# Kernel optimization log

Measured on AMD Instinct MI355X. Metric: run time of the kernel, lower is better.

Reference implementation:

```python
import jax, jax.numpy as jnp
import numpy as np

N, L, C, H, W, HEAD = 16, 256, 512, 32, 32, 16

def setup_inputs() -> dict:
    key = jax.random.key(0)
    ks = jax.random.split(key, 8)
    s = 0.02  # weight init scale
    return {
        "feature": jax.random.normal(ks[0], (N, C, H, W), jnp.float32),
        "token": jax.random.normal(ks[1], (N, L, C), jnp.float32),
        "wq": jax.random.normal(ks[2], (C, C), jnp.float32) * s,
        "bq": jax.random.normal(ks[3], (C,), jnp.float32) * s,
        "wk": jax.random.normal(ks[4], (C, C), jnp.float32) * s,
        "bk": jax.random.normal(ks[5], (C,), jnp.float32) * s,
        "wv": jax.random.normal(ks[6], (C, C), jnp.float32) * s,
        "bv": jax.random.normal(ks[7], (C,), jnp.float32) * s,
    }

def reference(feature, token, wq, bq, wk, bk, wv, bv):
    n, c, hgt, wid = feature.shape
    h = HEAD
    d = c // h
    l = token.shape[1]
    scale = jnp.asarray(np.sqrt(c / h), feature.dtype)
    tok = token.transpose(0, 2, 1)  # (N, C, L)
    # 1x1 conv projections == per-position GEMMs
    v = (jnp.einsum('ncl,dc->ndl', tok, wv) + bv[None, :, None]).reshape(n, h, d, l)
    k = (jnp.einsum('ncl,dc->ndl', tok, wk) + bk[None, :, None]).reshape(n, h, d, l)
    q = (jnp.einsum('nchw,dc->ndhw', feature, wq) + bq[None, :, None, None])
    q = q.reshape(n, h, d, hgt * wid).transpose(0, 1, 3, 2)  # (N, h, HW, d)
    scores = jnp.einsum('nhqd,nhdl->nhql', q, k) / scale  # (N, h, HW, L)
    coef = jax.nn.softmax(scores, axis=-1)
    proj = jnp.einsum('nhdl,nhql->nhdq', v, coef)  # (N, h, d, HW)
    return feature + proj.reshape(n, c, hgt, wid)
```

## Files before the change

### kernel.cpp

```cpp
#include <hip/hip_runtime.h>
#include <hip/hip_bf16.h>

#define N_ 16
#define L_ 256
#define C_ 512
#define HW_ 1024
#define HEADS_ 16
#define DH_ 32

typedef unsigned short u16;
typedef unsigned int u32;
typedef __attribute__((ext_vector_type(8))) short short8_t;
typedef __attribute__((ext_vector_type(4))) float f32x4;
typedef __attribute__((ext_vector_type(2))) unsigned int u32x2;

__device__ __forceinline__ u16 f2bs(float f) {
    union { float f; u32 i; } x; x.f = f;
    u32 r = x.i + 0x7fffu + ((x.i >> 16) & 1u);
    return (u16)(r >> 16);
}
__device__ __forceinline__ u32 cvt_pk_bf16(float lo, float hi) {
    u32 r;
    asm("v_cvt_pk_bf16_f32 %0, %1, %2" : "=v"(r) : "v"(lo), "v"(hi));
    return r;
}
#define AS1(p) (const __attribute__((address_space(1))) void*)(p)
#define AS3(p) (__attribute__((address_space(3))) void*)(p)

__global__ __launch_bounds__(256) void prep_kernel(
    const float* __restrict__ token, const float* __restrict__ wq,
    const float* __restrict__ wk, const float* __restrict__ wv,
    u16* __restrict__ tokb, u16* __restrict__ wqb,
    u16* __restrict__ wkb, u16* __restrict__ wvb)
{
    const int idx = blockIdx.x * 256 + threadIdx.x;
    const float* s; u16* d; int off;
    if (idx < 524288)            { s = token; d = tokb; off = idx; }
    else if (idx < 524288+65536) { s = wq; d = wqb; off = idx - 524288; }
    else if (idx < 524288+131072){ s = wk; d = wkb; off = idx - 524288 - 65536; }
    else                         { s = wv; d = wvb; off = idx - 524288 - 131072; }
    float4 v = ((const float4*)s)[off];
    ushort4 w;
    w.x = f2bs(v.x); w.y = f2bs(v.y); w.z = f2bs(v.z); w.w = f2bs(v.w);
    ((ushort4*)d)[off] = w;
}

__global__ __launch_bounds__(256) void proj_kernel(
    const float* __restrict__ feature,
    const u16* __restrict__ tokb, const u16* __restrict__ wqb,
    const u16* __restrict__ wkb, const u16* __restrict__ wvb,
    const float* __restrict__ bq, const float* __restrict__ bk,
    const float* __restrict__ bv,
    u16* __restrict__ Qout, u16* __restrict__ Kout, u16* __restrict__ Vt)
{
    __shared__ __align__(16) unsigned char smem[53248];

    const int t = threadIdx.x;
    const int lane = t & 63, wid = t >> 6;
    const int i16 = lane & 15, g = lane >> 4;

    if (blockIdx.x < 256) {
        const int xcd = blockIdx.x & 7, j = blockIdx.x >> 3;
        const int m0 = (xcd * 4 + (j & 3)) * 128;
        const int n0 = (j >> 2) * 64;
        u16* Tok = (u16*)smem;
        u16* Bk  = (u16*)(smem + 16384);
        u16* Bv  = (u16*)(smem + 24576);
        u16 (*LTo)[72] = (u16(*)[72])smem;

        const int wm = wid >> 1, wn = wid & 1;
        const int r8 = t >> 3, gr = t & 7;

        f32x4 ak[4][2], av[4][2];
        #pragma unroll
        for (int mt = 0; mt < 4; ++mt)
            #pragma unroll
            for (int nt = 0; nt < 2; ++nt) {
                ak[mt][nt] = (f32x4){0.f, 0.f, 0.f, 0.f};
                av[mt][nt] = (f32x4){0.f, 0.f, 0.f, 0.f};
            }

        for (int c0 = 0; c0 < C_; c0 += 64) {
            __syncthreads();
            #pragma unroll
            for (int p = 0; p < 4; ++p) {
                const int row = p * 32 + r8;
                __builtin_amdgcn_global_load_lds(
                    AS1(tokb + (size_t)(m0 + row) * C_ + c0 + ((gr ^ (row & 7)) << 3)),
                    AS3(smem + (p * 32 + wid * 8) * 128), 16, 0, 0);
            }
            #pragma unroll
            for (int p = 0; p < 2; ++p) {
                const int row = p * 32 + r8;
                const int gs = (gr ^ (row & 7)) << 3;
                __builtin_amdgcn_global_load_lds(
                    AS1(wkb + (size_t)(n0 + row) * C_ + c0 + gs),
                    AS3(smem + 16384 + (p * 32 + wid * 8) * 128), 16, 0, 0);
                __builtin_amdgcn_global_load_lds(
                    AS1(wvb + (size_t)(n0 + row) * C_ + c0 + gs),
                    AS3(smem + 24576 + (p * 32 + wid * 8) * 128), 16, 0, 0);
            }
            __syncthreads();
            #pragma unroll
            for (int ks = 0; ks < 2; ++ks) {
                short8_t a[4], bbk[2], bbv[2];
                #pragma unroll
                for (int mt = 0; mt < 4; ++mt) {
                    const int m = wm * 64 + mt * 16 + i16;
                    a[mt] = *(const short8_t*)&Tok[m * 64 + ((((ks << 2) | g) ^ (m & 7)) << 3)];
                }
                #pragma unroll
                for (int nt = 0; nt < 2; ++nt) {
                    const int d = wn * 32 + nt * 16 + i16;
                    const int sw = d * 64 + ((((ks << 2) | g) ^ (d & 7)) << 3);
                    bbk[nt] = *(const short8_t*)&Bk[sw];
                    bbv[nt] = *(const short8_t*)&Bv[sw];
                }
                #pragma unroll
                for (int mt = 0; mt < 4; ++mt)
                    #pragma unroll
                    for (int nt = 0; nt < 2; ++nt) {
                        ak[mt][nt] = __builtin_amdgcn_mfma_f32_16x16x32_bf16(
                            a[mt], bbk[nt], ak[mt][nt], 0, 0, 0);
                        av[mt][nt] = __builtin_amdgcn_mfma_f32_16x16x32_bf16(
                            a[mt], bbv[nt], av[mt][nt], 0, 0, 0);
                    }
            }
        }
        const int nb = m0 >> 8, l0 = m0 & 255;
        const size_t vtbase = (size_t)nb * C_ * L_;
        #pragma unroll
        for (int nt = 0; nt < 2; ++nt) {
            const int d = n0 + wn * 32 + nt * 16 + i16;
            const float bb = bv[d];
            #pragma unroll
            for (int mt = 0; mt < 4; ++mt) {
                ushort4 w;
                w.x = f2bs(av[mt][nt][0] + bb);
                w.y = f2bs(av[mt][nt][1] + bb);
                w.z = f2bs(av[mt][nt][2] + bb);
                w.w = f2bs(av[mt][nt][3] + bb);
                const int l = l0 + wm * 64 + mt * 16 + g * 4;
                *(ushort4*)&Vt[vtbase + (size_t)d * L_ + l] = w;
            }
        }
        __syncthreads();
        #pragma unroll
        for (int nt = 0; nt < 2; ++nt) {
            const int col = wn * 32 + nt * 16 + i16;
            const float bb = bk[n0 + col];
            #pragma unroll
            for (int mt = 0; mt < 4; ++mt)
                #pragma unroll
                for (int r = 0; r < 4; ++r)
                    LTo[wm * 64 + mt * 16 + g * 4 + r][col] = f2bs(ak[mt][nt][r] + bb);
        }
        __syncthreads();
        #pragma unroll
        for (int rep = 0; rep < 4; ++rep) {
            const int m = (t >> 3) + rep * 32;
            const int cs = (t & 7) * 8;
            *(short8_t*)&Kout[(size_t)(m0 + m) * C_ + n0 + cs] = *(short8_t*)&LTo[m][cs];
        }
    } else {
        const int qid = blockIdx.x - 256;
        const int xcd = qid & 7, loc = qid >> 3;
        const int mtile = xcd * 32 + (loc >> 2);
        const int nt4 = loc & 3;
        const int m0 = mtile * 64;
        const int n0 = nt4 * 128;
        const int n = m0 >> 10, pos0 = m0 & (HW_ - 1);
        const u32 FEAT0 = 32768;

        const int wq_d = wid & 1, wq_pos = wid >> 1;
        const int r8 = t >> 3, gr = t & 7;
        const int frow = t >> 2, fpb = t & 3;

        f32x4 acc[4][2];
        #pragma unroll
        for (int dm = 0; dm < 4; ++dm)
            #pragma unroll
            for (int pf = 0; pf < 2; ++pf)
                acc[dm][pf] = (f32x4){0.f, 0.f, 0.f, 0.f};

        float f[16];

        #define QF_LOADFEAT(c) { \
            const float* src = &feature[((size_t)n * C_ + (c) * 64 + frow) * HW_ + pos0 + fpb * 16]; \
            *(float4*)&f[0]  = *(const float4*)&src[0];  \
            *(float4*)&f[4]  = *(const float4*)&src[4];  \
            *(float4*)&f[8]  = *(const float4*)&src[8];  \
            *(float4*)&f[12] = *(const float4*)&src[12]; }
        #define QF_STAGEWQ(c, buf) { \
            _Pragma("unroll") \
            for (int p = 0; p < 4; ++p) { \
                const int row = p * 32 + r8; \
                __builtin_amdgcn_global_load_lds( \
                    AS1(wqb + (size_t)(n0 + row) * C_ + (c) * 64 + ((gr ^ (row & 7)) << 3)), \
                    AS3(smem + (buf) * 16384 + (p * 32 + wid * 8) * 128), 16, 0, 0); } }
        #define QF_WRITEFEAT(buf) { \
            u32 pw[8]; \
            _Pragma("unroll") \
            for (int k2 = 0; k2 < 8; ++k2) pw[k2] = cvt_pk_bf16(f[2*k2], f[2*k2+1]); \
            unsigned char* dst = smem + FEAT0 + (buf) * 10240 + \
                (u32)(((frow >> 2) * 4 + fpb) * 160 + (frow & 3) * 32); \
            *(short8_t*)dst = *(short8_t*)&pw[0]; \
            *(short8_t*)(dst + 16) = *(short8_t*)&pw[4]; }

        QF_LOADFEAT(0);
        QF_STAGEWQ(0, 0);
        QF_WRITEFEAT(0);
        __syncthreads();

        for (int c = 0; c < 8; ++c) {
            const int cur = c & 1;
            if (c < 7) {
                QF_LOADFEAT(c + 1);
                QF_STAGEWQ(c + 1, cur ^ 1);
            }
            short8_t a2[2][4], b2[2][2];
            #pragma unroll
            for (int ks = 0; ks < 2; ++ks)
                #pragma unroll
                for (int dm = 0; dm < 4; ++dm) {
                    const int m = wq_d * 64 + dm * 16 + i16;
                    a2[ks][dm] = *(const short8_t*)(smem + cur * 16384 +
                        (u32)(m * 128 + ((((ks << 2) | g) ^ (m & 7)) << 4)));
                }
            #pragma unroll
            for (int ks = 0; ks < 2; ++ks)
                #pragma unroll
                for (int pf = 0; pf < 2; ++pf) {
                    const int pb = wq_pos * 2 + pf;
                    const u32 vaddr = FEAT0 + cur * 10240 +
                        (u32)(((ks * 8 + g * 2) * 4 + pb) * 160) + (u32)i16 * 2;
                    u32x2 lo, hi;
                    asm volatile("ds_read_b64_tr_b16 %0, %1" : "=v"(lo) : "v"(vaddr));
                    asm volatile("ds_read_b64_tr_b16 %0, %1 offset:640" : "=v"(hi) : "v"(vaddr));
                    union { u32 w[4]; short8_t v; } pk;
                    pk.w[0] = lo[0]; pk.w[1] = lo[1];
                    pk.w[2] = hi[0]; pk.w[3] = hi[1];
                    b2[ks][pf] = pk.v;
                }
            asm volatile("s_waitcnt lgkmcnt(0)" ::: "memory");
            __builtin_amdgcn_sched_barrier(0);
            #pragma unroll
            for (int ks = 0; ks < 2; ++ks)
                #pragma unroll
                for (int dm = 0; dm < 4; ++dm)
                    #pragma unroll
                    for (int pf = 0; pf < 2; ++pf)
                        acc[dm][pf] = __builtin_amdgcn_mfma_f32_16x16x32_bf16(
                            a2[ks][dm], b2[ks][pf], acc[dm][pf], 0, 0, 0);
            if (c < 7) QF_WRITEFEAT(cur ^ 1);
            __syncthreads();
        }
        #pragma unroll
        for (int dm = 0; dm < 4; ++dm) {
            const int dbase = wq_d * 64 + dm * 16 + g * 4;
            float4 b4 = *(const float4*)&bq[n0 + dbase];
            const float bb[4] = {b4.x, b4.y, b4.z, b4.w};
            #pragma unroll
            for (int pf = 0; pf < 2; ++pf) {
                const int pos = wq_pos * 32 + pf * 16 + i16;
                ushort4 w;
                w.x = f2bs(acc[dm][pf][0] + bb[0]);
                w.y = f2bs(acc[dm][pf][1] + bb[1]);
                w.z = f2bs(acc[dm][pf][2] + bb[2]);
                w.w = f2bs(acc[dm][pf][3] + bb[3]);
                *(ushort4*)&Qout[(size_t)(m0 + pos) * C_ + n0 + dbase] = w;
            }
        }
    }
}

__global__ __launch_bounds__(256) void attn_kernel(
    const u16* __restrict__ Qws, const u16* __restrict__ Kws,
    const u16* __restrict__ Vws, const float* __restrict__ feature,
    float* __restrict__ out)
{
    __shared__ __align__(16) unsigned char smem[32768];

    const int t = threadIdx.x;
    const int wid = t >> 6, lane = t & 63;
    const int i16 = lane & 15, g = lane >> 4;
    const int pt = blockIdx.x, h = blockIdx.y, n = blockIdx.z;
    const int pos0 = pt * 64;
    const size_t qbase = ((size_t)n * HW_ + pos0) * C_ + h * DH_;
    const size_t kbase = ((size_t)n * L_) * C_ + h * DH_;
    const size_t vbase = (size_t)n * C_ * L_ + (size_t)h * DH_ * L_;

    const int q = wid * 16 + i16;

    short8_t bq = *(const short8_t*)&Qws[qbase + (size_t)q * C_ + g * 8];

    #pragma unroll
    for (int p = 0; p < 4; ++p) {
        const int kg = (lane & 3) ^ ((lane >> 3) & 3);
        const int kr = wid * 64 + p * 16 + (lane >> 2);
        const u16* ksrc = Kws + kbase + (size_t)kr * C_ + kg * 8;
        __builtin_amdgcn_global_load_lds(AS1(ksrc),
            AS3(smem + wid * 4096 + p * 1024), 16, 0, 0);
        const int vd = wid * 8 + p * 2 + (lane >> 5);
        const u16* vsrc = Vws + vbase + (size_t)vd * L_ + ((lane & 31) ^ (vd & 7)) * 8;
        __builtin_amdgcn_global_load_lds(AS1(vsrc),
            AS3(smem + 16384 + wid * 4096 + p * 1024), 16, 0, 0);
    }
    __syncthreads();

    const int kgr = g ^ ((i16 >> 1) & 3);
    f32x4 s[16];
    #pragma unroll
    for (int nf = 0; nf < 16; ++nf) {
        short8_t a = *(const short8_t*)(smem + (nf * 16 + i16) * 64 + kgr * 16);
        f32x4 z = {0.f, 0.f, 0.f, 0.f};
        s[nf] = __builtin_amdgcn_mfma_f32_16x16x32_bf16(a, bq, z, 0, 0, 0);
    }

    float mm[16], sm[16];
    #pragma unroll
    for (int nf = 0; nf < 16; ++nf)
        mm[nf] = fmaxf(fmaxf(s[nf][0], s[nf][1]), fmaxf(s[nf][2], s[nf][3]));
    #pragma unroll
    for (int st = 8; st >= 1; st >>= 1)
        #pragma unroll
        for (int i = 0; i < 8; ++i)
            if (i < st) mm[i] = fmaxf(mm[i], mm[i + st]);
    float m = mm[0];
    m = fmaxf(m, __shfl_xor(m, 16));
    m = fmaxf(m, __shfl_xor(m, 32));

    const float K2 = 0.25506288f;
    #pragma unroll
    for (int nf = 0; nf < 16; ++nf) {
        #pragma unroll
        for (int r = 0; r < 4; ++r) s[nf][r] = exp2f((s[nf][r] - m) * K2);
        sm[nf] = (s[nf][0] + s[nf][1]) + (s[nf][2] + s[nf][3]);
    }
    #pragma unroll
    for (int st = 8; st >= 1; st >>= 1)
        #pragma unroll
        for (int i = 0; i < 8; ++i)
            if (i < st) sm[i] += sm[i + st];
    float ssum = sm[0];
    ssum += __shfl_xor(ssum, 16);
    ssum += __shfl_xor(ssum, 32);
    const float pinv = 1.0f / ssum;

    __syncthreads();

    f32x4 o0 = {0.f, 0.f, 0.f, 0.f}, o1 = {0.f, 0.f, 0.f, 0.f};
    const int e7 = i16 & 7;

    #pragma unroll
    for (int hb = 0; hb < 2; ++hb) {
        #pragma unroll
        for (int nfp = 0; nfp < 8; ++nfp) {
            const int nf = hb * 8 + nfp;
            #pragma unroll
            for (int w = 0; w < 2; ++w) {
                u32 pw = cvt_pk_bf16(s[nf][2 * w] * pinv, s[nf][2 * w + 1] * pinv);
                const int gran = (nfp * 2 + (g >> 1)) ^ e7;
                *(u32*)(smem + q * 256 + gran * 16 + ((g & 1) * 2 + w) * 4) = pw;
            }
        }
        __syncthreads();
        #pragma unroll
        for (int ks = 0; ks < 4; ++ks) {
            short8_t pb = *(const short8_t*)(smem + q * 256 + (((ks * 4 + g) ^ e7) * 16));
            const int vg = (((hb * 4 + ks) * 4 + g) ^ e7) * 16;
            short8_t va0 = *(const short8_t*)(smem + 16384 + i16 * 512 + vg);
            short8_t va1 = *(const short8_t*)(smem + 16384 + (16 + i16) * 512 + vg);
            o0 = __builtin_amdgcn_mfma_f32_16x16x32_bf16(va0, pb, o0, 0, 0, 0);
            o1 = __builtin_amdgcn_mfma_f32_16x16x32_bf16(va1, pb, o1, 0, 0, 0);
        }
        if (hb == 0) __syncthreads();
    }

    const size_t obase = ((size_t)n * C_ + h * DH_) * HW_ + pos0 + q;
    #pragma unroll
    for (int r = 0; r < 4; ++r) {
        const size_t oa = obase + (size_t)(g * 4 + r) * HW_;
        out[oa] = feature[oa] + o0[r];
        const size_t ob = obase + (size_t)(16 + g * 4 + r) * HW_;
        out[ob] = feature[ob] + o1[r];
    }
}

extern "C" void kernel_launch(void* const* d_in, const int* in_sizes, int n_in,
                              void* d_out, int out_size, void* d_ws, size_t ws_size,
                              hipStream_t stream)
{
    const float* feature = (const float*)d_in[0];
    const float* token   = (const float*)d_in[1];
    const float* wq      = (const float*)d_in[2];
    const float* bq      = (const float*)d_in[3];
    const float* wk      = (const float*)d_in[4];
    const float* bk      = (const float*)d_in[5];
    const float* wv      = (const float*)d_in[6];
    const float* bv      = (const float*)d_in[7];
    float* out = (float*)d_out;

    u16* Qws = (u16*)d_ws;
    u16* Kws = Qws + (size_t)N_ * HW_ * C_;
    u16* Vws = Kws + (size_t)N_ * L_ * C_;

    char* ob = (char*)d_out;
    u16* tokb = (u16*)(ob + (16u << 20));
    u16* wkb  = (u16*)(ob + (20u << 20));
    u16* wvb  = (u16*)(ob + (20u << 20) + 524288);
    u16* wqb  = (u16*)(ob + (21u << 20));

    prep_kernel<<<dim3(2816), 256, 0, stream>>>(token, wq, wk, wv,
                                                tokb, wqb, wkb, wvb);
    proj_kernel<<<dim3(1280), 256, 0, stream>>>(feature, tokb, wqb, wkb, wvb,
                                                bq, bk, bv, Qws, Kws, Vws);
    attn_kernel<<<dim3(16, 16, 16), 256, 0, stream>>>(Qws, Kws, Vws, feature, out);
}
```

Measured before the change: 72.89 us.

## Double-buffer feature register prefetch two stages ahead in Q projection loop

```diff
diff --git a/kernel.cpp b/kernel.cpp
--- a/kernel.cpp
+++ b/kernel.cpp
@@ -183,14 +183,14 @@
             for (int pf = 0; pf < 2; ++pf)
                 acc[dm][pf] = (f32x4){0.f, 0.f, 0.f, 0.f};
 
-        float f[16];
-
-        #define QF_LOADFEAT(c) { \
+        float fA[16], fB[16];
+
+        #define QF_LOADFEAT(dstf, c) { \
             const float* src = &feature[((size_t)n * C_ + (c) * 64 + frow) * HW_ + pos0 + fpb * 16]; \
-            *(float4*)&f[0]  = *(const float4*)&src[0];  \
-            *(float4*)&f[4]  = *(const float4*)&src[4];  \
-            *(float4*)&f[8]  = *(const float4*)&src[8];  \
-            *(float4*)&f[12] = *(const float4*)&src[12]; }
+            *(float4*)&dstf[0]  = *(const float4*)&src[0];  \
+            *(float4*)&dstf[4]  = *(const float4*)&src[4];  \
+            *(float4*)&dstf[8]  = *(const float4*)&src[8];  \
+            *(float4*)&dstf[12] = *(const float4*)&src[12]; }
         #define QF_STAGEWQ(c, buf) { \
             _Pragma("unroll") \
             for (int p = 0; p < 4; ++p) { \
@@ -198,62 +198,80 @@
                 __builtin_amdgcn_global_load_lds( \
                     AS1(wqb + (size_t)(n0 + row) * C_ + (c) * 64 + ((gr ^ (row & 7)) << 3)), \
                     AS3(smem + (buf) * 16384 + (p * 32 + wid * 8) * 128), 16, 0, 0); } }
-        #define QF_WRITEFEAT(buf) { \
+        #define QF_WRITEFEAT(srcf, buf) { \
             u32 pw[8]; \
             _Pragma("unroll") \
-            for (int k2 = 0; k2 < 8; ++k2) pw[k2] = cvt_pk_bf16(f[2*k2], f[2*k2+1]); \
+            for (int k2 = 0; k2 < 8; ++k2) pw[k2] = cvt_pk_bf16(srcf[2*k2], srcf[2*k2+1]); \
             unsigned char* dst = smem + FEAT0 + (buf) * 10240 + \
                 (u32)(((frow >> 2) * 4 + fpb) * 160 + (frow & 3) * 32); \
             *(short8_t*)dst = *(short8_t*)&pw[0]; \
             *(short8_t*)(dst + 16) = *(short8_t*)&pw[4]; }
-
-        QF_LOADFEAT(0);
+        #define QF_COMPUTE(buf) { \
+            short8_t a2[2][4], b2[2][2]; \
+            _Pragma("unroll") \
+            for (int ks = 0; ks < 2; ++ks) \
+                _Pragma("unroll") \
+                for (int dm = 0; dm < 4; ++dm) { \
+                    const int m_ = wq_d * 64 + dm * 16 + i16; \
+                    a2[ks][dm] = *(const short8_t*)(smem + (buf) * 16384 + \
+                        (u32)(m_ * 128 + ((((ks << 2) | g) ^ (m_ & 7)) << 4))); } \
+            _Pragma("unroll") \
+            for (int ks = 0; ks < 2; ++ks) \
+                _Pragma("unroll") \
+                for (int pf = 0; pf < 2; ++pf) { \
+                    const int pb = wq_pos * 2 + pf; \
+                    const u32 vaddr = FEAT0 + (buf) * 10240 + \
+                        (u32)(((ks * 8 + g * 2) * 4 + pb) * 160) + (u32)i16 * 2; \
+                    u32x2 lo, hi; \
+                    asm volatile("ds_read_b64_tr_b16 %0, %1" : "=v"(lo) : "v"(vaddr)); \
+                    asm volatile("ds_read_b64_tr_b16 %0, %1 offset:640" : "=v"(hi) : "v"(vaddr)); \
+                    union { u32 w[4]; short8_t v; } pk; \
+                    pk.w[0] = lo[0]; pk.w[1] = lo[1]; \
+                    pk.w[2] = hi[0]; pk.w[3] = hi[1]; \
+                    b2[ks][pf] = pk.v; } \
+            asm volatile("s_waitcnt lgkmcnt(0)" ::: "memory"); \
+            __builtin_amdgcn_sched_barrier(0); \
+            _Pragma("unroll") \
+            for (int ks = 0; ks < 2; ++ks) \
+                _Pragma("unroll") \
+                for (int dm = 0; dm < 4; ++dm) \
+                    _Pragma("unroll") \
+                    for (int pf = 0; pf < 2; ++pf) \
+                        acc[dm][pf] = __builtin_amdgcn_mfma_f32_16x16x32_bf16( \
+                            a2[ks][dm], b2[ks][pf], acc[dm][pf], 0, 0, 0); }
+
         QF_STAGEWQ(0, 0);
-        QF_WRITEFEAT(0);
-        __syncthreads();
-
+        __builtin_amdgcn_sched_barrier(0);
+        QF_LOADFEAT(fA, 0);
+        QF_LOADFEAT(fB, 1);
+        __builtin_amdgcn_sched_barrier(0);
+        QF_WRITEFEAT(fA, 0);
+        asm volatile("s_waitcnt lgkmcnt(0)" ::: "memory");
+        __builtin_amdgcn_sched_barrier(0);
+        __builtin_amdgcn_s_barrier();
+
+        #pragma unroll
         for (int c = 0; c < 8; ++c) {
             const int cur = c & 1;
             if (c < 7) {
-                QF_LOADFEAT(c + 1);
                 QF_STAGEWQ(c + 1, cur ^ 1);
-            }
-            short8_t a2[2][4], b2[2][2];
-            #pragma unroll
-            for (int ks = 0; ks < 2; ++ks)
-                #pragma unroll
-                for (int dm = 0; dm < 4; ++dm) {
-                    const int m = wq_d * 64 + dm * 16 + i16;
-                    a2[ks][dm] = *(const short8_t*)(smem + cur * 16384 +
-                        (u32)(m * 128 + ((((ks << 2) | g) ^ (m & 7)) << 4)));
-                }
-            #pragma unroll
-            for (int ks = 0; ks < 2; ++ks)
-                #pragma unroll
-                for (int pf = 0; pf < 2; ++pf) {
-                    const int pb = wq_pos * 2 + pf;
-                    const u32 vaddr = FEAT0 + cur * 10240 +
-                        (u32)(((ks * 8 + g * 2) * 4 + pb) * 160) + (u32)i16 * 2;
-                    u32x2 lo, hi;
-                    asm volatile("ds_read_b64_tr_b16 %0, %1" : "=v"(lo) : "v"(vaddr));
-                    asm volatile("ds_read_b64_tr_b16 %0, %1 offset:640" : "=v"(hi) : "v"(vaddr));
-                    union { u32 w[4]; short8_t v; } pk;
-                    pk.w[0] = lo[0]; pk.w[1] = lo[1];
-                    pk.w[2] = hi[0]; pk.w[3] = hi[1];
-                    b2[ks][pf] = pk.v;
-                }
-            asm volatile("s_waitcnt lgkmcnt(0)" ::: "memory");
-            __builtin_amdgcn_sched_barrier(0);
-            #pragma unroll
-            for (int ks = 0; ks < 2; ++ks)
-                #pragma unroll
-                for (int dm = 0; dm < 4; ++dm)
-                    #pragma unroll
-                    for (int pf = 0; pf < 2; ++pf)
-                        acc[dm][pf] = __builtin_amdgcn_mfma_f32_16x16x32_bf16(
-                            a2[ks][dm], b2[ks][pf], acc[dm][pf], 0, 0, 0);
-            if (c < 7) QF_WRITEFEAT(cur ^ 1);
-            __syncthreads();
+                __builtin_amdgcn_sched_barrier(0);
+            }
+            if (c < 6) {
+                if ((c & 1) == 0) { QF_LOADFEAT(fA, c + 2); }
+                else              { QF_LOADFEAT(fB, c + 2); }
+                __builtin_amdgcn_sched_barrier(0);
+            }
+            QF_COMPUTE(cur);
+            if (c < 7) {
+                if ((c & 1) == 0) { QF_WRITEFEAT(fB, cur ^ 1); }
+                else              { QF_WRITEFEAT(fA, cur ^ 1); }
+                if (c < 6) { asm volatile("s_waitcnt vmcnt(4)" ::: "memory"); }
+                else       { asm volatile("s_waitcnt vmcnt(0)" ::: "memory"); }
+                asm volatile("s_waitcnt lgkmcnt(0)" ::: "memory");
+                __builtin_amdgcn_sched_barrier(0);
+                __builtin_amdgcn_s_barrier();
+            }
         }
         #pragma unroll
         for (int dm = 0; dm < 4; ++dm) {
```

New measurement: 72.68 us. Within noise of the previous version (-0.3%).
